# Kernel tuning notes

Hardware: AMD Instinct MI355X
Metric: run time of the kernel (lower is better)

Reference implementation:

```python
import jax, jax.numpy as jnp
import numpy as np

D_MODEL = 1024
N_HEADS = 16
HEAD_DIM = D_MODEL // N_HEADS


def setup_inputs() -> dict:
    key = jax.random.key(0)
    k_x, k_qkv, k_proj = jax.random.split(key, 3)
    x = jax.random.normal(k_x, (2, 2048, D_MODEL), dtype=jnp.float32)
    # flax nnx.Linear kernels: shape (in_features, out_features), lecun_normal-ish scale
    w_qkv = jax.random.normal(k_qkv, (D_MODEL, 3 * D_MODEL), dtype=jnp.float32) / np.sqrt(D_MODEL)
    w_proj = jax.random.normal(k_proj, (D_MODEL, D_MODEL), dtype=jnp.float32) / np.sqrt(D_MODEL)
    return {"x": x, "w_qkv": w_qkv, "w_proj": w_proj}


def reference(x, w_qkv, w_proj):
    bsz, seq_len, d_model = x.shape
    qkv = x @ w_qkv  # (B, T, 3*D)
    q, k, v = jnp.split(qkv, 3, axis=-1)
    q = q.reshape(bsz, seq_len, N_HEADS, HEAD_DIM)
    k = k.reshape(bsz, seq_len, N_HEADS, HEAD_DIM)
    v = v.reshape(bsz, seq_len, N_HEADS, HEAD_DIM)
    scale = jnp.sqrt(jnp.asarray(HEAD_DIM, dtype=x.dtype))
    attn_logits = jnp.einsum('bthd,bshd->bhts', q / scale, k)  # (B, H, T, T)
    attn_weights = jax.nn.softmax(attn_logits, axis=-1)
    attn_out = jnp.einsum('bhts,bshd->bthd', attn_weights, v)
    attn_out = attn_out.reshape(bsz, seq_len, d_model)
    return attn_out @ w_proj
```

## Files before the change

kernel.cpp:

```cpp
#include <hip/hip_runtime.h>
#include <hip/hip_bf16.h>
#include <cmath>

#define D_MODEL 1024
#define NH 16
#define HD 64
#define BSZ 2
#define SEQ 2048
#define MTOT (BSZ * SEQ)

typedef _Float16 f16x8 __attribute__((ext_vector_type(8)));
typedef __fp16   fp16x2 __attribute__((ext_vector_type(2)));
typedef float    f32x4  __attribute__((ext_vector_type(4)));
typedef float    f32x16 __attribute__((ext_vector_type(16)));

#define QSCALE 0.18033688011112042f

__device__ __forceinline__ ushort f2h(float x) {
    union { _Float16 h; ushort u; } cv;
    cv.h = (_Float16)x;
    return cv.u;
}
__device__ __forceinline__ uint pkh(float a, float b) {
    union { fp16x2 h; uint u; } cv;
    cv.h = __builtin_amdgcn_cvt_pkrtz(a, b);
    return cv.u;
}
__device__ __forceinline__ float fexp2(float x) {
    float r; asm("v_exp_f32 %0, %1" : "=v"(r) : "v"(x)); return r;
}
__device__ __forceinline__ void gload_lds16(const ushort* g, ushort* l) {
    __builtin_amdgcn_global_load_lds(
        (const __attribute__((address_space(1))) void*)g,
        (__attribute__((address_space(3))) void*)l, 16, 0, 0);
}

__global__ __launch_bounds__(256)
void cast8(const float* __restrict__ in, ushort* __restrict__ out, int n)
{
    const int i = (blockIdx.x * 256 + threadIdx.x) * 8;
    if (i >= n) return;
    float4 a = *(const float4*)(in + i);
    float4 b = *(const float4*)(in + i + 4);
    alignas(16) ushort h8[8];
    h8[0] = f2h(a.x); h8[1] = f2h(a.y); h8[2] = f2h(a.z); h8[3] = f2h(a.w);
    h8[4] = f2h(b.x); h8[5] = f2h(b.y); h8[6] = f2h(b.z); h8[7] = f2h(b.w);
    *(uint4*)(out + i) = *(const uint4*)h8;
}

__global__ __launch_bounds__(256)
void transpose_cast(const float* __restrict__ in, ushort* __restrict__ out,
                    int R, int C)
{
    __shared__ float tile[32][33];
    const int t  = threadIdx.x;
    const int r0 = blockIdx.y * 32, c0 = blockIdx.x * 32;
    const int tr = t >> 5, tc = t & 31;
#pragma unroll
    for (int s = 0; s < 4; ++s)
        tile[tr + 8 * s][tc] = in[(size_t)(r0 + tr + 8 * s) * C + c0 + tc];
    __syncthreads();
#pragma unroll
    for (int s = 0; s < 4; ++s)
        out[(size_t)(c0 + tr + 8 * s) * R + r0 + tc] = f2h(tile[tc][tr + 8 * s]);
}

template <int MODE>
__global__ __launch_bounds__(256)
void gemm_mfma(const ushort* __restrict__ A, const ushort* __restrict__ Bt,
               float* __restrict__ outp,
               ushort* __restrict__ Qw, ushort* __restrict__ Kw,
               ushort* __restrict__ Vw, int N)
{
    __shared__ ushort As[128 * 64];
    __shared__ ushort Bs[128 * 64];

    const int t  = threadIdx.x;
    const int w  = t >> 6;
    const int l  = t & 63;
    const int lr = l & 15;
    const int lg = l >> 4;
    const int wr = w >> 1, wc = w & 1;
    const int m0 = blockIdx.y * 128, n0 = blockIdx.x * 128;

    const int srow = l >> 3;
    const int scol = (l & 7) * 8;

    const ushort* Ab = A  + (size_t)m0 * 1024;
    const ushort* Bb = Bt + (size_t)n0 * 1024;

    f32x4 acc[4][4];
#pragma unroll
    for (int i = 0; i < 4; ++i)
#pragma unroll
        for (int j = 0; j < 4; ++j) acc[i][j] = (f32x4){0.f, 0.f, 0.f, 0.f};

    for (int k0 = 0; k0 < 1024; k0 += 64) {
#pragma unroll
        for (int i = 0; i < 4; ++i) {
            const int r8 = (w * 4 + i) * 8;
            gload_lds16(Ab + (size_t)(r8 + srow) * 1024 + k0 + scol, &As[r8 * 64]);
            gload_lds16(Bb + (size_t)(r8 + srow) * 1024 + k0 + scol, &Bs[r8 * 64]);
        }
        __syncthreads();

#pragma unroll
        for (int kk = 0; kk < 2; ++kk) {
            f16x8 af[4], bf[4];
#pragma unroll
            for (int m = 0; m < 4; ++m)
                af[m] = *(const f16x8*)&As[(wr * 64 + m * 16 + lr) * 64 + kk * 32 + lg * 8];
#pragma unroll
            for (int n = 0; n < 4; ++n)
                bf[n] = *(const f16x8*)&Bs[(wc * 64 + n * 16 + lr) * 64 + kk * 32 + lg * 8];
#pragma unroll
            for (int m = 0; m < 4; ++m)
#pragma unroll
                for (int n = 0; n < 4; ++n)
                    acc[m][n] = __builtin_amdgcn_mfma_f32_16x16x32_f16(
                        af[m], bf[n], acc[m][n], 0, 0, 0);
        }
        __syncthreads();
    }

    if (MODE == 1) {
#pragma unroll
        for (int mf = 0; mf < 4; ++mf) {
            const int row = m0 + wr * 64 + mf * 16 + lg * 4;
#pragma unroll
            for (int nf = 0; nf < 4; ++nf) {
                const int col = n0 + wc * 64 + nf * 16 + lr;
#pragma unroll
                for (int i = 0; i < 4; ++i)
                    outp[(size_t)(row + i) * N + col] = acc[mf][nf][i];
            }
        }
    } else {
#pragma unroll
        for (int mf = 0; mf < 4; ++mf) {
            const int row = m0 + wr * 64 + mf * 16 + lg * 4;
            const int b   = row >> 11;
            const int tt0 = row & (SEQ - 1);
#pragma unroll
            for (int nf = 0; nf < 4; ++nf) {
                const int col   = n0 + wc * 64 + nf * 16 + lr;
                const int which = col >> 10;
                const int h     = (col >> 6) & 15;
                const int d     = col & 63;
                ushort* dst = (which == 0) ? Qw : (which == 1) ? Kw : Vw;
                const float sc = (which == 0) ? QSCALE : 1.0f;
#pragma unroll
                for (int i = 0; i < 4; ++i)
                    dst[((size_t)(b * NH + h) * SEQ + tt0 + i) * HD + d] =
                        f2h(acc[mf][nf][i] * sc);
            }
        }
    }
}

__global__ __launch_bounds__(256)
void attn_mfma2(const ushort* __restrict__ Qw, const ushort* __restrict__ Kw,
                const ushort* __restrict__ Vw, ushort* __restrict__ AO)
{
    __shared__ ushort Ks[2][64 * 64];
    __shared__ ushort Vt[2][64 * 64];

    const int t  = threadIdx.x;
    const int w  = t >> 6;
    const int l  = t & 63;
    const int q  = l & 31;
    const int hi = l >> 5;

    const int bh = blockIdx.y;
    const int q0 = blockIdx.x * 128 + w * 32;

    const ushort* Qp = Qw + (size_t)bh * SEQ * HD;
    const ushort* Kp = Kw + (size_t)bh * SEQ * HD;
    const ushort* Vp = Vw + (size_t)bh * SEQ * HD;

    f16x8 qf[4];
#pragma unroll
    for (int kc = 0; kc < 4; ++kc)
        qf[kc] = *(const f16x8*)(Qp + (size_t)(q0 + q) * HD + kc * 16 + hi * 8);

    f32x16 oacc[2];
#pragma unroll
    for (int db = 0; db < 2; ++db)
#pragma unroll
        for (int r = 0; r < 16; ++r) oacc[db][r] = 0.f;
    float m_run = -3.0e38f, l_run = 0.f;

    auto stageK = [&](int buf, int k0) {
#pragma unroll
        for (int s = 0; s < 2; ++s) {
            const int c    = w * 64 + l + 256 * s;
            const int row  = c >> 3;
            const int unit = (c & 7) ^ (row & 7);
            gload_lds16(Kp + (size_t)(k0 + row) * HD + unit * 8,
                        &Ks[buf][(w * 64 + 256 * s) * 8]);
        }
    };
    const int vkey = l;
    auto loadV = [&](int k0, uint4& r0, uint4& r1) {
        r0 = *(const uint4*)(Vp + (size_t)(k0 + vkey) * HD + w * 8);
        r1 = *(const uint4*)(Vp + (size_t)(k0 + vkey) * HD + (w + 4) * 8);
    };
    auto writeV = [&](int buf, uint4 r0, uint4 r1) {
        alignas(16) ushort e8[8];
        *(uint4*)e8 = r0;
#pragma unroll
        for (int i = 0; i < 8; ++i) {
            const int d = w * 8 + i;
            *(ushort*)((char*)Vt[buf] + (d * 128 + ((vkey * 2) ^ (i << 4)))) = e8[i];
        }
        *(uint4*)e8 = r1;
#pragma unroll
        for (int i = 0; i < 8; ++i) {
            const int d = (w + 4) * 8 + i;
            *(ushort*)((char*)Vt[buf] + (d * 128 + ((vkey * 2) ^ (i << 4)))) = e8[i];
        }
    };

    {
        uint4 r0, r1;
        stageK(0, 0);
        loadV(0, r0, r1);
        writeV(0, r0, r1);
    }
    __syncthreads();

    int cur = 0;
    for (int kt = 0; kt < SEQ / 64; ++kt) {
        const bool pf = (kt + 1 < SEQ / 64);
        uint4 vr0, vr1;
        if (pf) {
            stageK(cur ^ 1, (kt + 1) * 64);
            loadV((kt + 1) * 64, vr0, vr1);
        }

        f32x16 sacc[2];
#pragma unroll
        for (int kb = 0; kb < 2; ++kb) {
            f32x16 a;
#pragma unroll
            for (int r = 0; r < 16; ++r) a[r] = 0.f;
            const int row = kb * 32 + q;
            const int swz = (row & 7) << 4;
#pragma unroll
            for (int kc = 0; kc < 4; ++kc) {
                f16x8 kf = *(const f16x8*)(
                    (const char*)Ks[cur] + row * 128 + ((kc * 32 + hi * 16) ^ swz));
                a = __builtin_amdgcn_mfma_f32_32x32x16_f16(kf, qf[kc], a, 0, 0, 0);
            }
            sacc[kb] = a;
        }

        float tm[16];
#pragma unroll
        for (int r = 0; r < 16; ++r) tm[r] = fmaxf(sacc[0][r], sacc[1][r]);
#pragma unroll
        for (int s = 8; s > 0; s >>= 1)
#pragma unroll
            for (int r = 0; r < 8; ++r)
                if (r < s) tm[r] = fmaxf(tm[r], tm[r + s]);
        float mx = fmaxf(tm[0], __shfl_xor(tm[0], 32));
        const float m_new = fmaxf(m_run, mx);
        const float scale = fexp2(m_run - m_new);
        m_run = m_new;

#pragma unroll
        for (int kb = 0; kb < 2; ++kb)
#pragma unroll
            for (int r = 0; r < 16; ++r)
                sacc[kb][r] = fexp2(sacc[kb][r] - m_new);

        float ts[16];
#pragma unroll
        for (int r = 0; r < 16; ++r) ts[r] = sacc[0][r] + sacc[1][r];
#pragma unroll
        for (int s = 8; s > 0; s >>= 1)
#pragma unroll
            for (int r = 0; r < 8; ++r)
                if (r < s) ts[r] += ts[r + s];
        float sum = ts[0] + __shfl_xor(ts[0], 32);
        l_run = l_run * scale + sum;
#pragma unroll
        for (int db = 0; db < 2; ++db)
#pragma unroll
            for (int r = 0; r < 16; ++r) oacc[db][r] *= scale;

        f16x8 pfrag[4];
#pragma unroll
        for (int kb = 0; kb < 2; ++kb)
#pragma unroll
            for (int lc = 0; lc < 2; ++lc) {
                const int rb = lc * 8;
                uint a = pkh(sacc[kb][rb + 0], sacc[kb][rb + 1]);
                uint b = pkh(sacc[kb][rb + 2], sacc[kb][rb + 3]);
                uint c = pkh(sacc[kb][rb + 4], sacc[kb][rb + 5]);
                uint d = pkh(sacc[kb][rb + 6], sacc[kb][rb + 7]);
                uint xa = __shfl_xor(a, 32), xb = __shfl_xor(b, 32);
                uint xc = __shfl_xor(c, 32), xd = __shfl_xor(d, 32);
                union { uint u[4]; f16x8 v; } f;
                f.u[0] = hi ? xc : a;
                f.u[1] = hi ? xd : b;
                f.u[2] = hi ? c : xa;
                f.u[3] = hi ? d : xb;
                pfrag[kb * 2 + lc] = f.v;
            }

#pragma unroll
        for (int db = 0; db < 2; ++db) {
            const int row = db * 32 + q;
            const int swz = (row & 7) << 4;
#pragma unroll
            for (int kc = 0; kc < 4; ++kc) {
                f16x8 vf = *(const f16x8*)(
                    (const char*)Vt[cur] + row * 128 + ((kc * 32 + hi * 16) ^ swz));
                oacc[db] = __builtin_amdgcn_mfma_f32_32x32x16_f16(
                    vf, pfrag[kc], oacc[db], 0, 0, 0);
            }
        }

        if (pf) writeV(cur ^ 1, vr0, vr1);
        __syncthreads();
        cur ^= 1;
    }

    const float inv = 1.f / l_run;
    const int b = bh >> 4, h = bh & 15;
    ushort* orow = AO + ((size_t)(b * SEQ) + q0 + q) * D_MODEL + h * HD;
#pragma unroll
    for (int db = 0; db < 2; ++db)
#pragma unroll
        for (int g = 0; g < 4; ++g) {
            const int d = db * 32 + g * 8 + hi * 4;
            alignas(8) ushort e4[4];
#pragma unroll
            for (int i = 0; i < 4; ++i) e4[i] = f2h(oacc[db][g * 4 + i] * inv);
            *(uint2*)(orow + d) = *(const uint2*)e4;
        }
}

extern "C" void kernel_launch(void* const* d_in, const int* in_sizes, int n_in,
                              void* d_out, int out_size, void* d_ws, size_t ws_size,
                              hipStream_t stream)
{
    const float* x      = (const float*)d_in[0];
    const float* w_qkv  = (const float*)d_in[1];
    const float* w_proj = (const float*)d_in[2];
    float* out = (float*)d_out;

    ushort* Xh  = (ushort*)d_ws;
    ushort* WqT = Xh  + (size_t)MTOT * D_MODEL;
    ushort* WpT = WqT + (size_t)3 * D_MODEL * D_MODEL;
    ushort* Qw  = WpT + (size_t)D_MODEL * D_MODEL;
    ushort* Kw  = Qw  + (size_t)MTOT * D_MODEL;
    ushort* Vw  = Kw  + (size_t)MTOT * D_MODEL;
    ushort* AOh = Vw  + (size_t)MTOT * D_MODEL;

    dim3 blk(256);

    cast8<<<dim3(MTOT * D_MODEL / (8 * 256)), blk, 0, stream>>>(x, Xh, MTOT * D_MODEL);
    transpose_cast<<<dim3(3 * D_MODEL / 32, D_MODEL / 32), blk, 0, stream>>>(
        w_qkv, WqT, D_MODEL, 3 * D_MODEL);
    transpose_cast<<<dim3(D_MODEL / 32, D_MODEL / 32), blk, 0, stream>>>(
        w_proj, WpT, D_MODEL, D_MODEL);

    gemm_mfma<0><<<dim3(3 * D_MODEL / 128, MTOT / 128), blk, 0, stream>>>(
        Xh, WqT, nullptr, Qw, Kw, Vw, 3 * D_MODEL);

    attn_mfma2<<<dim3(SEQ / 128, BSZ * NH), blk, 0, stream>>>(Qw, Kw, Vw, AOh);

    gemm_mfma<1><<<dim3(D_MODEL / 128, MTOT / 128), blk, 0, stream>>>(
        AOh, WpT, out, nullptr, nullptr, nullptr, D_MODEL);
}
```

Measured before the change: 158.5 us.

## Split attention KV range across two warp groups and merge partial softmax states

After: 151.5 us. 4.4% less time.

```diff
diff --git a/kernel.cpp b/kernel.cpp
--- a/kernel.cpp
+++ b/kernel.cpp
@@ -158,26 +158,33 @@
     }
 }
 
-__global__ __launch_bounds__(256)
-void attn_mfma2(const ushort* __restrict__ Qw, const ushort* __restrict__ Kw,
+__global__ __launch_bounds__(512, 4)
+void attn_mfma3(const ushort* __restrict__ Qw, const ushort* __restrict__ Kw,
                 const ushort* __restrict__ Vw, ushort* __restrict__ AO)
 {
-    __shared__ ushort Ks[2][64 * 64];
-    __shared__ ushort Vt[2][64 * 64];
-
-    const int t  = threadIdx.x;
-    const int w  = t >> 6;
-    const int l  = t & 63;
-    const int q  = l & 31;
-    const int hi = l >> 5;
+    __shared__ ushort KsAll[2][2][64 * 64];
+    __shared__ ushort VtAll[2][2][64 * 64];
+
+    const int t    = threadIdx.x;
+    const int w    = t >> 6;
+    const int l    = t & 63;
+    const int q    = l & 31;
+    const int hi   = l >> 5;
+    const int half = w >> 2;
+    const int ww   = w & 3;
 
     const int bh = blockIdx.y;
-    const int q0 = blockIdx.x * 128 + w * 32;
+    const int q0 = blockIdx.x * 128 + ww * 32;
+    const int kbase = half * (SEQ / 2);
+    const int NT = (SEQ / 2) / 64;
 
     const ushort* Qp = Qw + (size_t)bh * SEQ * HD;
     const ushort* Kp = Kw + (size_t)bh * SEQ * HD;
     const ushort* Vp = Vw + (size_t)bh * SEQ * HD;
 
+    ushort (*Ks)[64 * 64] = KsAll[half];
+    ushort (*Vt)[64 * 64] = VtAll[half];
+
     f16x8 qf[4];
 #pragma unroll
     for (int kc = 0; kc < 4; ++kc)
@@ -193,52 +200,53 @@
     auto stageK = [&](int buf, int k0) {
 #pragma unroll
         for (int s = 0; s < 2; ++s) {
-            const int c    = w * 64 + l + 256 * s;
+            const int c    = ww * 64 + l + 256 * s;
             const int row  = c >> 3;
             const int unit = (c & 7) ^ (row & 7);
             gload_lds16(Kp + (size_t)(k0 + row) * HD + unit * 8,
-                        &Ks[buf][(w * 64 + 256 * s) * 8]);
+                        &Ks[buf][(ww * 64 + 256 * s) * 8]);
         }
     };
     const int vkey = l;
     auto loadV = [&](int k0, uint4& r0, uint4& r1) {
-        r0 = *(const uint4*)(Vp + (size_t)(k0 + vkey) * HD + w * 8);
-        r1 = *(const uint4*)(Vp + (size_t)(k0 + vkey) * HD + (w + 4) * 8);
+        r0 = *(const uint4*)(Vp + (size_t)(k0 + vkey) * HD + ww * 8);
+        r1 = *(const uint4*)(Vp + (size_t)(k0 + vkey) * HD + (ww + 4) * 8);
     };
     auto writeV = [&](int buf, uint4 r0, uint4 r1) {
         alignas(16) ushort e8[8];
         *(uint4*)e8 = r0;
 #pragma unroll
         for (int i = 0; i < 8; ++i) {
-            const int d = w * 8 + i;
+            const int d = ww * 8 + i;
             *(ushort*)((char*)Vt[buf] + (d * 128 + ((vkey * 2) ^ (i << 4)))) = e8[i];
         }
         *(uint4*)e8 = r1;
 #pragma unroll
         for (int i = 0; i < 8; ++i) {
-            const int d = (w + 4) * 8 + i;
+            const int d = (ww + 4) * 8 + i;
             *(ushort*)((char*)Vt[buf] + (d * 128 + ((vkey * 2) ^ (i << 4)))) = e8[i];
         }
     };
 
     {
         uint4 r0, r1;
-        stageK(0, 0);
-        loadV(0, r0, r1);
+        stageK(0, kbase);
+        loadV(kbase, r0, r1);
         writeV(0, r0, r1);
     }
     __syncthreads();
 
     int cur = 0;
-    for (int kt = 0; kt < SEQ / 64; ++kt) {
-        const bool pf = (kt + 1 < SEQ / 64);
+    for (int kt = 0; kt < NT; ++kt) {
+        const bool pf = (kt + 1 < NT);
         uint4 vr0, vr1;
         if (pf) {
-            stageK(cur ^ 1, (kt + 1) * 64);
-            loadV((kt + 1) * 64, vr0, vr1);
+            stageK(cur ^ 1, kbase + (kt + 1) * 64);
+            loadV(kbase + (kt + 1) * 64, vr0, vr1);
         }
 
         f32x16 sacc[2];
+        __builtin_amdgcn_s_setprio(1);
 #pragma unroll
         for (int kb = 0; kb < 2; ++kb) {
             f32x16 a;
@@ -254,6 +262,7 @@
             }
             sacc[kb] = a;
         }
+        __builtin_amdgcn_s_setprio(0);
 
         float tm[16];
 #pragma unroll
@@ -264,15 +273,23 @@
             for (int r = 0; r < 8; ++r)
                 if (r < s) tm[r] = fmaxf(tm[r], tm[r + s]);
         float mx = fmaxf(tm[0], __shfl_xor(tm[0], 32));
-        const float m_new = fmaxf(m_run, mx);
-        const float scale = fexp2(m_run - m_new);
-        m_run = m_new;
+
+        if (__any(mx > m_run + 8.0f)) {
+            const float m_new = fmaxf(m_run, mx);
+            const float scale = fexp2(m_run - m_new);
+            m_run = m_new;
+            l_run *= scale;
+#pragma unroll
+            for (int db = 0; db < 2; ++db)
+#pragma unroll
+                for (int r = 0; r < 16; ++r) oacc[db][r] *= scale;
+        }
 
 #pragma unroll
         for (int kb = 0; kb < 2; ++kb)
 #pragma unroll
             for (int r = 0; r < 16; ++r)
-                sacc[kb][r] = fexp2(sacc[kb][r] - m_new);
+                sacc[kb][r] = fexp2(sacc[kb][r] - m_run);
 
         float ts[16];
 #pragma unroll
@@ -282,12 +299,7 @@
 #pragma unroll
             for (int r = 0; r < 8; ++r)
                 if (r < s) ts[r] += ts[r + s];
-        float sum = ts[0] + __shfl_xor(ts[0], 32);
-        l_run = l_run * scale + sum;
-#pragma unroll
-        for (int db = 0; db < 2; ++db)
-#pragma unroll
-            for (int r = 0; r < 16; ++r) oacc[db][r] *= scale;
+        l_run += ts[0] + __shfl_xor(ts[0], 32);
 
         f16x8 pfrag[4];
 #pragma unroll
@@ -309,6 +321,7 @@
                 pfrag[kb * 2 + lc] = f.v;
             }
 
+        __builtin_amdgcn_s_setprio(1);
 #pragma unroll
         for (int db = 0; db < 2; ++db) {
             const int row = db * 32 + q;
@@ -321,25 +334,51 @@
                     vf, pfrag[kc], oacc[db], 0, 0, 0);
             }
         }
+        __builtin_amdgcn_s_setprio(0);
 
         if (pf) writeV(cur ^ 1, vr0, vr1);
         __syncthreads();
         cur ^= 1;
     }
 
-    const float inv = 1.f / l_run;
-    const int b = bh >> 4, h = bh & 15;
-    ushort* orow = AO + ((size_t)(b * SEQ) + q0 + q) * D_MODEL + h * HD;
-#pragma unroll
-    for (int db = 0; db < 2; ++db)
-#pragma unroll
-        for (int g = 0; g < 4; ++g) {
-            const int d = db * 32 + g * 8 + hi * 4;
-            alignas(8) ushort e4[4];
-#pragma unroll
-            for (int i = 0; i < 4; ++i) e4[i] = f2h(oacc[db][g * 4 + i] * inv);
-            *(uint2*)(orow + d) = *(const uint2*)e4;
-        }
+    float* oex = (float*)KsAll;
+    float* mex = (float*)VtAll;
+    float* lex = mex + 256;
+
+    if (half == 1) {
+        mex[ww * 64 + l] = m_run;
+        lex[ww * 64 + l] = l_run;
+#pragma unroll
+        for (int db = 0; db < 2; ++db)
+#pragma unroll
+            for (int r = 0; r < 16; ++r)
+                oex[(((ww * 2 + db) * 16) + r) * 64 + l] = oacc[db][r];
+    }
+    __syncthreads();
+    if (half == 0) {
+        const float m2 = mex[ww * 64 + l];
+        const float l2 = lex[ww * 64 + l];
+        const float mf = fmaxf(m_run, m2);
+        float w1 = fexp2(m_run - mf), w2 = fexp2(m2 - mf);
+        const float inv = 1.f / (l_run * w1 + l2 * w2);
+        w1 *= inv; w2 *= inv;
+
+        const int b = bh >> 4, h = bh & 15;
+        ushort* orow = AO + ((size_t)(b * SEQ) + q0 + q) * D_MODEL + h * HD;
+#pragma unroll
+        for (int db = 0; db < 2; ++db)
+#pragma unroll
+            for (int g = 0; g < 4; ++g) {
+                const int d = db * 32 + g * 8 + hi * 4;
+                alignas(8) ushort e4[4];
+#pragma unroll
+                for (int i = 0; i < 4; ++i) {
+                    const float o2 = oex[(((ww * 2 + db) * 16) + g * 4 + i) * 64 + l];
+                    e4[i] = f2h(oacc[db][g * 4 + i] * w1 + o2 * w2);
+                }
+                *(uint2*)(orow + d) = *(const uint2*)e4;
+            }
+    }
 }
 
 extern "C" void kernel_launch(void* const* d_in, const int* in_sizes, int n_in,
@@ -370,7 +409,7 @@
     gemm_mfma<0><<<dim3(3 * D_MODEL / 128, MTOT / 128), blk, 0, stream>>>(
         Xh, WqT, nullptr, Qw, Kw, Vw, 3 * D_MODEL);
 
-    attn_mfma2<<<dim3(SEQ / 128, BSZ * NH), blk, 0, stream>>>(Qw, Kw, Vw, AOh);
+    attn_mfma3<<<dim3(SEQ / 128, BSZ * NH), dim3(512), 0, stream>>>(Qw, Kw, Vw, AOh);
 
     gemm_mfma<1><<<dim3(D_MODEL / 128, MTOT / 128), blk, 0, stream>>>(
         AOh, WpT, out, nullptr, nullptr, nullptr, D_MODEL);
```
